# Kernel tuning notes

Measured on AMD Instinct MI355X. Metric: run time of the kernel, lower is better.

Reference implementation:

```python
import jax, jax.numpy as jnp
import numpy as np

B, T, N, H = 64, 512, 1024, 1024


def setup_inputs() -> dict:
    key = jax.random.key(0)
    k = jax.random.split(key, 6)
    s = 1.0 / np.sqrt(H)
    return {
        "x": jax.random.normal(k[0], (B, T, N), dtype=jnp.float32),
        "mix": jax.random.uniform(k[1], (B, T, 1), dtype=jnp.float32),
        "W_ih": jax.random.uniform(k[2], (3 * H, N), minval=-s, maxval=s, dtype=jnp.float32),
        "W_hh": jax.random.uniform(k[3], (3 * H, H), minval=-s, maxval=s, dtype=jnp.float32),
        "b_ih": jax.random.uniform(k[4], (3 * H,), minval=-s, maxval=s, dtype=jnp.float32),
        "b_hh": jax.random.uniform(k[5], (3 * H,), minval=-s, maxval=s, dtype=jnp.float32),
    }


def reference(x, mix, W_ih, W_hh, b_ih, b_hh):
    # PyTorch GRUCell gate order: r, z, n
    Hs = W_hh.shape[1]
    # Precompute input projections for all steps: [B,T,3H]
    xW = jnp.einsum("btn,kn->btk", x, W_ih) + b_ih
    xr, xz, xn = jnp.split(xW, 3, axis=-1)
    # time-major for scan
    xs = (jnp.swapaxes(xr, 0, 1), jnp.swapaxes(xz, 0, 1), jnp.swapaxes(xn, 0, 1),
          jnp.swapaxes(mix, 0, 1))
    h0 = jnp.zeros((x.shape[0], Hs), dtype=x.dtype)

    def step(h, inp):
        xr_t, xz_t, xn_t, m_t = inp
        hW = h @ W_hh.T + b_hh  # [B,3H]
        hr, hz, hn = jnp.split(hW, 3, axis=-1)
        r = jax.nn.sigmoid(xr_t + hr)
        z = jax.nn.sigmoid(xz_t + hz)
        n = jnp.tanh(xn_t + r * hn)
        h_new = (1.0 - z) * n + z * h
        h_mix = h_new * m_t + h * (1.0 - m_t)  # skip-mix blend
        return h_mix, h_mix

    o, h_hist = jax.lax.scan(step, h0, xs)
    h = jnp.swapaxes(h_hist, 0, 1)  # [B,T,H]
    return h, o
```

## Files before the change

### kernel.cpp

```cpp
#include <hip/hip_runtime.h>

typedef _Float16 f16;
typedef __attribute__((ext_vector_type(4))) _Float16 f16x4;
typedef __attribute__((ext_vector_type(8))) _Float16 f16x8;
typedef __attribute__((ext_vector_type(4))) float f32x4;

#define NT 512

__global__ __launch_bounds__(256) void gemm_xw(
    const float* __restrict__ x,
    const float* __restrict__ Wih,
    f16* __restrict__ xw)
{
  const int nblk = blockIdx.x;
  const int mblk = blockIdx.y;
  const int tid  = threadIdx.x;
  const int lane = tid & 63;
  const int wv   = tid >> 6;
  const int wm   = wv >> 1;
  const int wn   = wv & 1;

  __shared__ f16 sA[128 * 40];
  __shared__ f16 sB[128 * 40];

  const int m0 = mblk * 128;
  const int n0 = nblk * 128;

  const int srow = tid >> 3;
  const int scol = (tid & 7) * 4;

  const int lr = lane & 15;
  const int lk = (lane >> 4) * 8;

  f32x4 acc[4][4];
#pragma unroll
  for (int i = 0; i < 4; ++i)
#pragma unroll
    for (int jj = 0; jj < 4; ++jj) acc[i][jj] = (f32x4){0.f, 0.f, 0.f, 0.f};

  for (int kb = 0; kb < 32; ++kb) {
    const int k0 = kb * 32;
#pragma unroll
    for (int rb = 0; rb < 4; ++rb) {
      const int row = srow + rb * 32;
      float4 va = *(const float4*)&x[(size_t)(m0 + row) * 1024 + k0 + scol];
      f16x4 ha; ha[0] = va.x; ha[1] = va.y; ha[2] = va.z; ha[3] = va.w;
      *(f16x4*)&sA[row * 40 + scol] = ha;
      float4 vb = *(const float4*)&Wih[(size_t)(n0 + row) * 1024 + k0 + scol];
      f16x4 hb; hb[0] = vb.x; hb[1] = vb.y; hb[2] = vb.z; hb[3] = vb.w;
      *(f16x4*)&sB[row * 40 + scol] = hb;
    }
    __syncthreads();
    f16x8 af[4], bfr[4];
#pragma unroll
    for (int mi = 0; mi < 4; ++mi)
      af[mi] = *(const f16x8*)&sA[(wm * 64 + mi * 16 + lr) * 40 + lk];
#pragma unroll
    for (int ni = 0; ni < 4; ++ni)
      bfr[ni] = *(const f16x8*)&sB[(wn * 64 + ni * 16 + lr) * 40 + lk];
#pragma unroll
    for (int mi = 0; mi < 4; ++mi)
#pragma unroll
      for (int ni = 0; ni < 4; ++ni)
        acc[mi][ni] = __builtin_amdgcn_mfma_f32_16x16x32_f16(af[mi], bfr[ni], acc[mi][ni], 0, 0, 0);
    __syncthreads();
  }

  const int b  = mblk >> 2;
  const int t0 = (mblk & 3) * 128;
  const int g  = nblk >> 3;
  const int j0 = (nblk & 7) * 128;
#pragma unroll
  for (int mi = 0; mi < 4; ++mi) {
#pragma unroll
    for (int r = 0; r < 4; ++r) {
      const int ri = wm * 64 + mi * 16 + (lane >> 4) * 4 + r;
      const int t  = t0 + ri;
#pragma unroll
      for (int ni = 0; ni < 4; ++ni) {
        const int j = j0 + wn * 64 + ni * 16 + lr;
        xw[(size_t)((t * 3 + g) * 64 + b) * 1024 + j] = (f16)acc[mi][ni][r];
      }
    }
  }
}

__device__ __forceinline__ float sigm(float v) { return 1.f / (1.f + __expf(-v)); }
__device__ __forceinline__ float tanh_fast(float v) { return 1.f - 2.f / (1.f + __expf(2.f * v)); }

__global__ __launch_bounds__(192, 1) void recur(
    const f16* __restrict__ xw,
    const float* __restrict__ mixp,
    const float* __restrict__ Whh,
    const float* __restrict__ bih,
    const float* __restrict__ bhh,
    float* __restrict__ out,
    f16* __restrict__ hbuf,
    int* __restrict__ flags)
{
  const int c = blockIdx.x;
  const int m = blockIdx.y;
  const int tid = threadIdx.x;
  const int w = tid >> 6;
  const int lane = tid & 63;
  const int lr = lane & 15;
  const int q  = lane >> 4;
  const int lk = q * 8;
  const int rrow = q * 4;
  const int m0 = m * 16;
  const int j  = c * 16 + lr;
  const int grow = w * 1024 + j;

  __shared__ float smix[16][512];
  __shared__ f16 hstage[16 * 1040];
  __shared__ float ldsRZ[2][16][16];
  __shared__ f16 ldsH[16 * 16];
  __shared__ float ldsO[2][16 * 16];
  __shared__ int stokA, stokB;

  if (tid == 0) { stokA = 0; stokB = 0; }
  for (int i = tid; i < 2048; i += 192) {
    const int row = i >> 7;
    const int col = (i & 127) * 4;
    *(float4*)&smix[row][col] = *(const float4*)&mixp[(m0 + row) * 512 + col];
  }

  f16x8 bf[32];
#pragma unroll
  for (int kc = 0; kc < 32; ++kc) {
    const float* s = &Whh[(size_t)grow * 1024 + kc * 32 + lk];
    float4 v0 = *(const float4*)(s);
    float4 v1 = *(const float4*)(s + 4);
    f16x8 hv;
    hv[0] = v0.x; hv[1] = v0.y; hv[2] = v0.z; hv[3] = v0.w;
    hv[4] = v1.x; hv[5] = v1.y; hv[6] = v1.z; hv[7] = v1.w;
    bf[kc] = hv;
  }
  const float bhw = bhh[grow];
  float bi0 = 0.f, bi1 = 0.f, bi2 = 0.f;
  if (w == 2) { bi0 = bih[j]; bi1 = bih[1024 + j]; bi2 = bih[2048 + j]; }

  float hprev[4] = {0.f, 0.f, 0.f, 0.f};
  int* cnt = &flags[m * 8 * 32];

  __syncthreads();

  float xr[4], xz[4], xn[4], mt[4];
  if (w == 2) {
#pragma unroll
    for (int r = 0; r < 4; ++r) {
      const int b = m0 + rrow + r;
      xr[r] = (float)__builtin_nontemporal_load(&xw[(size_t)(0 * 64 + b) * 1024 + j]);
      xz[r] = (float)__builtin_nontemporal_load(&xw[(size_t)(1 * 64 + b) * 1024 + j]);
      xn[r] = (float)__builtin_nontemporal_load(&xw[(size_t)(2 * 64 + b) * 1024 + j]);
      mt[r] = smix[rrow + r][0];
    }
  }

  for (int t = 0; t < NT; ++t) {
    if (t > 0 && w < 2) {
      if (w == 0 && c == 0 && lane == 0 && t >= 2)
        __hip_atomic_store(&cnt[((t - 2) & 7) * 32], 0,
                           __ATOMIC_RELAXED, __HIP_MEMORY_SCOPE_AGENT);
      while (__hip_atomic_load(&cnt[(t & 7) * 32], __ATOMIC_RELAXED,
                               __HIP_MEMORY_SCOPE_AGENT) < 64) {}
      asm volatile("" ::: "memory");
      const f16* hsrc = hbuf + (size_t)(t & 1) * (64 * 1024) + (size_t)m0 * 1024;
      f16x8 v[16];
#pragma unroll
      for (int i = 0; i < 16; ++i) {
        const int row = 2 * (i & 7) + (lane >> 5);
        const int ch  = w * 64 + (i >> 3) * 32 + (lane & 31);
        const f16* p = hsrc + row * 1024 + ch * 8;
        asm volatile("global_load_dwordx4 %0, %1, off sc0 sc1"
                     : "=v"(v[i]) : "v"(p));
      }
      if (w == 1) {
        f32x4 ov = *(const f32x4*)&ldsO[(t - 1) & 1][(lane >> 2) * 16 + (lane & 3) * 4];
        float* pa = out + ((size_t)(m0 + (lane >> 2)) * 512 + (t - 1)) * 1024 + c * 16 + (lane & 3) * 4;
        asm volatile("global_store_dwordx4 %0, %1, off nt"
                     :: "v"(pa), "v"(ov) : "memory");
        asm volatile("s_waitcnt vmcnt(1)" ::: "memory");
      } else {
        asm volatile("s_waitcnt vmcnt(0)" ::: "memory");
      }
#pragma unroll
      for (int i = 0; i < 16; ++i) {
        asm volatile("" : "+v"(v[i]));
        const int row = 2 * (i & 7) + (lane >> 5);
        const int ch  = w * 64 + (i >> 3) * 32 + (lane & 31);
        *(f16x8*)&hstage[row * 1040 + ((ch ^ (row & 7)) * 8)] = v[i];
      }
      asm volatile("s_waitcnt lgkmcnt(0)" ::: "memory");
      if (lane == 0) { if (w == 0) *(volatile int*)&stokA = t; else *(volatile int*)&stokB = t; }
    }
    f32x4 acc = {0.f, 0.f, 0.f, 0.f};
    if (t > 0) {
      f32x4 a0 = {0,0,0,0}, a1 = {0,0,0,0}, a2 = {0,0,0,0}, a3 = {0,0,0,0};
      if (w != 0) { while (*(volatile int*)&stokA < t) {} }
      asm volatile("" ::: "memory");
      __builtin_amdgcn_sched_barrier(0);
#pragma unroll
      for (int kc = 0; kc < 16; kc += 4) {
        f16x8 h0 = *(const f16x8*)&hstage[lr * 1040 + ((((kc + 0) * 4 + q) ^ (lr & 7)) * 8)];
        f16x8 h1 = *(const f16x8*)&hstage[lr * 1040 + ((((kc + 1) * 4 + q) ^ (lr & 7)) * 8)];
        f16x8 h2 = *(const f16x8*)&hstage[lr * 1040 + ((((kc + 2) * 4 + q) ^ (lr & 7)) * 8)];
        f16x8 h3 = *(const f16x8*)&hstage[lr * 1040 + ((((kc + 3) * 4 + q) ^ (lr & 7)) * 8)];
        a0 = __builtin_amdgcn_mfma_f32_16x16x32_f16(h0, bf[kc + 0], a0, 0, 0, 0);
        a1 = __builtin_amdgcn_mfma_f32_16x16x32_f16(h1, bf[kc + 1], a1, 0, 0, 0);
        a2 = __builtin_amdgcn_mfma_f32_16x16x32_f16(h2, bf[kc + 2], a2, 0, 0, 0);
        a3 = __builtin_amdgcn_mfma_f32_16x16x32_f16(h3, bf[kc + 3], a3, 0, 0, 0);
      }
      if (w != 1) { while (*(volatile int*)&stokB < t) {} }
      asm volatile("" ::: "memory");
      __builtin_amdgcn_sched_barrier(0);
#pragma unroll
      for (int kc = 16; kc < 32; kc += 4) {
        f16x8 h0 = *(const f16x8*)&hstage[lr * 1040 + ((((kc + 0) * 4 + q) ^ (lr & 7)) * 8)];
        f16x8 h1 = *(const f16x8*)&hstage[lr * 1040 + ((((kc + 1) * 4 + q) ^ (lr & 7)) * 8)];
        f16x8 h2 = *(const f16x8*)&hstage[lr * 1040 + ((((kc + 2) * 4 + q) ^ (lr & 7)) * 8)];
        f16x8 h3 = *(const f16x8*)&hstage[lr * 1040 + ((((kc + 3) * 4 + q) ^ (lr & 7)) * 8)];
        a0 = __builtin_amdgcn_mfma_f32_16x16x32_f16(h0, bf[kc + 0], a0, 0, 0, 0);
        a1 = __builtin_amdgcn_mfma_f32_16x16x32_f16(h1, bf[kc + 1], a1, 0, 0, 0);
        a2 = __builtin_amdgcn_mfma_f32_16x16x32_f16(h2, bf[kc + 2], a2, 0, 0, 0);
        a3 = __builtin_amdgcn_mfma_f32_16x16x32_f16(h3, bf[kc + 3], a3, 0, 0, 0);
      }
      acc = (a0 + a1) + (a2 + a3);
    }
    if (w < 2) {
#pragma unroll
      for (int r = 0; r < 4; ++r) ldsRZ[w][rrow + r][lr] = acc[r] + bhw;
    }
    __syncthreads();
    if (w == 2) {
      float* lo = &ldsO[t & 1][0];
#pragma unroll
      for (int r = 0; r < 4; ++r) {
        const int row = rrow + r;
        const float hr = ldsRZ[0][row][lr];
        const float hz = ldsRZ[1][row][lr];
        const float hn = acc[r] + bhw;
        const float rg = sigm(xr[r] + bi0 + hr);
        const float zg = sigm(xz[r] + bi1 + hz);
        const float ng = tanh_fast(xn[r] + bi2 + rg * hn);
        const float hnew = (1.f - zg) * ng + zg * hprev[r];
        const float hm = mt[r] * hnew + (1.f - mt[r]) * hprev[r];
        hprev[r] = hm;
        ldsH[row * 16 + lr] = (f16)hm;
        lo[row * 16 + lr] = hm;
      }
      asm volatile("s_waitcnt lgkmcnt(0)" ::: "memory");
      if (lane < 32) {
        f16x8 hv = *(const f16x8*)&ldsH[(lane >> 1) * 16 + (lane & 1) * 8];
        f16* p = hbuf + (size_t)((t + 1) & 1) * (64 * 1024)
               + (size_t)(m0 + (lane >> 1)) * 1024 + c * 16 + (lane & 1) * 8;
        asm volatile("global_store_dwordx4 %0, %1, off sc0 sc1"
                     :: "v"(p), "v"(hv) : "memory");
      }
      asm volatile("s_waitcnt vmcnt(0) lgkmcnt(0)" ::: "memory");
      if (lane == 0)
        __hip_atomic_fetch_add(&cnt[((t + 1) & 7) * 32], 1,
                               __ATOMIC_RELAXED, __HIP_MEMORY_SCOPE_AGENT);
      const int tn = (t + 1 < NT) ? t + 1 : NT - 1;
#pragma unroll
      for (int r = 0; r < 4; ++r) {
        const int b = m0 + rrow + r;
        xr[r] = (float)__builtin_nontemporal_load(&xw[(size_t)((tn * 3 + 0) * 64 + b) * 1024 + j]);
        xz[r] = (float)__builtin_nontemporal_load(&xw[(size_t)((tn * 3 + 1) * 64 + b) * 1024 + j]);
        xn[r] = (float)__builtin_nontemporal_load(&xw[(size_t)((tn * 3 + 2) * 64 + b) * 1024 + j]);
        mt[r] = smix[rrow + r][tn];
      }
    }
  }
  __syncthreads();
  if (w == 1) {
    const int row = lane >> 2, part = lane & 3;
    f32x4 ov = *(const f32x4*)&ldsO[1][row * 16 + part * 4];
    float* p1 = out + ((size_t)(m0 + row) * 512 + 511) * 1024 + c * 16 + part * 4;
    float* p2 = out + (size_t)64 * 512 * 1024 + (size_t)(m0 + row) * 1024 + c * 16 + part * 4;
    __builtin_nontemporal_store(ov, (f32x4*)p1);
    __builtin_nontemporal_store(ov, (f32x4*)p2);
  }
}

extern "C" void kernel_launch(void* const* d_in, const int* in_sizes, int n_in,
                              void* d_out, int out_size, void* d_ws, size_t ws_size,
                              hipStream_t stream) {
  const float* x    = (const float*)d_in[0];
  const float* mixp = (const float*)d_in[1];
  const float* Wih  = (const float*)d_in[2];
  const float* Whh  = (const float*)d_in[3];
  const float* bih  = (const float*)d_in[4];
  const float* bhh  = (const float*)d_in[5];
  float* out = (float*)d_out;

  const size_t XW_BYTES = (size_t)512 * 3 * 64 * 1024 * sizeof(f16);
  f16* xw    = (f16*)d_ws;
  f16* hbuf  = (f16*)((char*)d_ws + XW_BYTES);
  int* flags = (int*)((char*)d_ws + XW_BYTES + (size_t)2 * 64 * 1024 * sizeof(f16));

  hipMemsetAsync(flags, 0, 4096, stream);

  dim3 gg(24, 256);
  gemm_xw<<<gg, 256, 0, stream>>>(x, Wih, xw);

  dim3 gr(64, 4);
  recur<<<gr, 192, 0, stream>>>(xw, mixp, Whh, bih, bhh, out, hbuf, flags);
}
```

Measured before the change: 2.501 ms.

## Replace atomic counter barrier with per-block flags and aggregated epoch broadcast

The per-step grid barrier among the 64 column blocks of each batch group used a shared atomic counter that every block incremented and polled, plus a rolling reset. Now each block stores its step number into its own padded flag. Block c==0 gathers all 64 flags with one wavefront, publishes the epoch to 16 padded slots, and signals its second wave through LDS. Other blocks poll a spread-out epoch slot, which aims to cut atomic contention and same-line polling traffic at the cost of an extra hop through the aggregator block.

```diff
diff --git a/kernel.cpp b/kernel.cpp
--- a/kernel.cpp
+++ b/kernel.cpp
@@ -116,9 +116,9 @@
   __shared__ float ldsRZ[2][16][16];
   __shared__ f16 ldsH[16 * 16];
   __shared__ float ldsO[2][16 * 16];
-  __shared__ int stokA, stokB;
-
-  if (tid == 0) { stokA = 0; stokB = 0; }
+  __shared__ int stokA, stokB, ldsTok;
+
+  if (tid == 0) { stokA = 0; stokB = 0; ldsTok = 0; }
   for (int i = tid; i < 2048; i += 192) {
     const int row = i >> 7;
     const int col = (i & 127) * 4;
@@ -141,7 +141,9 @@
   if (w == 2) { bi0 = bih[j]; bi1 = bih[1024 + j]; bi2 = bih[2048 + j]; }
 
   float hprev[4] = {0.f, 0.f, 0.f, 0.f};
-  int* cnt = &flags[m * 8 * 32];
+  int* gbase  = &flags[m * 4096];
+  int* myflag = &gbase[c * 32];
+  int* epoch  = &gbase[2048];
 
   __syncthreads();
 
@@ -159,11 +161,23 @@
 
   for (int t = 0; t < NT; ++t) {
     if (t > 0 && w < 2) {
-      if (w == 0 && c == 0 && lane == 0 && t >= 2)
-        __hip_atomic_store(&cnt[((t - 2) & 7) * 32], 0,
-                           __ATOMIC_RELAXED, __HIP_MEMORY_SCOPE_AGENT);
-      while (__hip_atomic_load(&cnt[(t & 7) * 32], __ATOMIC_RELAXED,
-                               __HIP_MEMORY_SCOPE_AGENT) < 64) {}
+      if (c == 0) {
+        if (w == 0) {
+          while (__hip_atomic_load(&gbase[lane * 32], __ATOMIC_RELAXED,
+                                   __HIP_MEMORY_SCOPE_AGENT) < t) {}
+          __builtin_amdgcn_sched_barrier(0);
+          if (lane < 16)
+            __hip_atomic_store(&epoch[lane * 32], t,
+                               __ATOMIC_RELAXED, __HIP_MEMORY_SCOPE_AGENT);
+          *(volatile int*)&ldsTok = t;
+        } else {
+          while (*(volatile int*)&ldsTok < t) {}
+        }
+      } else {
+        int* ep = &epoch[((c & 7) + 8 * w) * 32];
+        while (__hip_atomic_load(ep, __ATOMIC_RELAXED,
+                                 __HIP_MEMORY_SCOPE_AGENT) < t) {}
+      }
       asm volatile("" ::: "memory");
       const f16* hsrc = hbuf + (size_t)(t & 1) * (64 * 1024) + (size_t)m0 * 1024;
       f16x8 v[16];
@@ -259,8 +273,7 @@
       }
       asm volatile("s_waitcnt vmcnt(0) lgkmcnt(0)" ::: "memory");
       if (lane == 0)
-        __hip_atomic_fetch_add(&cnt[((t + 1) & 7) * 32], 1,
-                               __ATOMIC_RELAXED, __HIP_MEMORY_SCOPE_AGENT);
+        __hip_atomic_store(myflag, t + 1, __ATOMIC_RELAXED, __HIP_MEMORY_SCOPE_AGENT);
       const int tn = (t + 1 < NT) ? t + 1 : NT - 1;
 #pragma unroll
       for (int r = 0; r < 4; ++r) {
@@ -299,7 +312,7 @@
   f16* hbuf  = (f16*)((char*)d_ws + XW_BYTES);
   int* flags = (int*)((char*)d_ws + XW_BYTES + (size_t)2 * 64 * 1024 * sizeof(f16));
 
-  hipMemsetAsync(flags, 0, 4096, stream);
+  hipMemsetAsync(flags, 0, 4 * 4096 * sizeof(int), stream);
 
   dim3 gg(24, 256);
   gemm_xw<<<gg, 256, 0, stream>>>(x, Wih, xw);
```

Measured after the change: 2.582 ms. +3.2%, slower.
